# Kernel tuning notes

Hardware: AMD Instinct MI355X
Metric: run time of the kernel (lower is better)

## Reference

```python
import jax, jax.numpy as jnp
import numpy as np

EPS = 1e-5

def _layer_norm(x, w, b):
    mu = jnp.mean(x, axis=-1, keepdims=True)
    var = jnp.mean(jnp.square(x - mu), axis=-1, keepdims=True)
    return (x - mu) * jax.lax.rsqrt(var + EPS) * w + b

def setup_inputs() -> dict:
    key = jax.random.key(0)
    ks = jax.random.split(key, 8)
    B, S, D = 8, 2048, 1024
    image_features = jax.random.normal(ks[0], (B, S, D), dtype=jnp.float32)
    text_features = jax.random.normal(ks[1], (B, S, D), dtype=jnp.float32)
    ln_w = jnp.ones((D,), dtype=jnp.float32)
    ln_b = jnp.zeros((D,), dtype=jnp.float32)
    lim = 1.0 / np.sqrt(D)
    W_img = jax.random.uniform(ks[2], (D, D), minval=-lim, maxval=lim, dtype=jnp.float32)
    b_img = jax.random.uniform(ks[3], (D,), minval=-lim, maxval=lim, dtype=jnp.float32)
    W_txt = jax.random.uniform(ks[4], (D, D), minval=-lim, maxval=lim, dtype=jnp.float32)
    b_txt = jax.random.uniform(ks[5], (D,), minval=-lim, maxval=lim, dtype=jnp.float32)
    return {"image_features": image_features, "text_features": text_features,
            "ln_w": ln_w, "ln_b": ln_b, "W_img": W_img, "b_img": b_img,
            "W_txt": W_txt, "b_txt": b_txt}

def reference(image_features, text_features, ln_w, ln_b, W_img, b_img, W_txt, b_txt):
    D = image_features.shape[-1]
    scale = D ** (-0.5)
    image_norm = _layer_norm(image_features, ln_w, ln_b)
    text_norm = _layer_norm(text_features, ln_w, ln_b)
    # torch Linear: x @ W^T + b
    image_proj = jnp.einsum('bsd,ed->bse', image_norm, W_img) + b_img  # [B,Si,D]
    text_proj = jnp.einsum('btd,ed->bte', text_norm, W_txt) + b_txt    # [B,St,D]
    attn = jnp.einsum('bsd,btd->bst', image_proj, text_proj) * scale   # [B,Si,St]
    attn = jax.nn.softmax(attn, axis=-1)
    image_out = jnp.einsum('bst,btd->bsd', attn, text_proj)            # [B,Si,D]
    text_out = jnp.einsum('bst,bsd->btd', attn, image_proj)            # [B,St,D]
    return (image_out, text_out)
```

## Files before the change

kernel.cpp:

```cpp
#include <hip/hip_runtime.h>


#define DEV __device__ __forceinline__

typedef short s16x8 __attribute__((ext_vector_type(8)));
typedef float f32x4 __attribute__((ext_vector_type(4)));

DEV unsigned short f2bf(float f){
  unsigned u = __float_as_uint(f);
  u = (u + 0x7fffu + ((u >> 16) & 1u)) >> 16;
  return (unsigned short)u;
}
DEV float bf2f(unsigned short s){ return __uint_as_float(((unsigned)s) << 16); }

DEV void ldsload16(const void* g, void* l){
  __builtin_amdgcn_global_load_lds((const __attribute__((address_space(1))) void*)g,
                                   (__attribute__((address_space(3))) void*)l, 16, 0, 0);
}

__global__ __launch_bounds__(256) void k_cvt(const float* __restrict__ src,
                                             unsigned short* __restrict__ dst, int n4){
  int i = blockIdx.x * 256 + threadIdx.x;
  if (i < n4){
    float4 v = ((const float4*)src)[i];
    ushort4 o;
    o.x = f2bf(v.x); o.y = f2bf(v.y); o.z = f2bf(v.z); o.w = f2bf(v.w);
    ((ushort4*)dst)[i] = o;
  }
}

__global__ __launch_bounds__(256) void k_ln(const float* __restrict__ x,
                                            const float* __restrict__ w,
                                            const float* __restrict__ b,
                                            unsigned short* __restrict__ y){
  int row = blockIdx.x, tid = threadIdx.x;
  float4 v = ((const float4*)(x + (size_t)row * 1024))[tid];
  float s  = v.x + v.y + v.z + v.w;
  float s2 = v.x*v.x + v.y*v.y + v.z*v.z + v.w*v.w;
  #pragma unroll
  for (int o = 32; o > 0; o >>= 1){ s += __shfl_xor(s, o, 64); s2 += __shfl_xor(s2, o, 64); }
  __shared__ float sh[8];
  int wv = tid >> 6, ln = tid & 63;
  if (!ln){ sh[wv] = s; sh[4 + wv] = s2; }
  __syncthreads();
  s  = sh[0] + sh[1] + sh[2] + sh[3];
  s2 = sh[4] + sh[5] + sh[6] + sh[7];
  float mean = s * (1.f/1024.f);
  float var  = s2 * (1.f/1024.f) - mean * mean;
  float rstd = rsqrtf(var + 1e-5f);
  float4 w4 = ((const float4*)w)[tid];
  float4 b4 = ((const float4*)b)[tid];
  ushort4 o;
  o.x = f2bf((v.x-mean)*rstd*w4.x + b4.x);
  o.y = f2bf((v.y-mean)*rstd*w4.y + b4.y);
  o.z = f2bf((v.z-mean)*rstd*w4.z + b4.z);
  o.w = f2bf((v.w-mean)*rstd*w4.w + b4.w);
  ((ushort4*)(y + (size_t)row * 1024))[tid] = o;
}

#define STG(MAT, BASE, LD, T, H) do{                                              \
  ldsload16((BASE) + (size_t)(rl      ) * (LD) + (T)*64 + (H)*32 + g8,            \
            &MAT[(T)&1][H][(wave*16)*32]);                                        \
  ldsload16((BASE) + (size_t)(rl + 128) * (LD) + (T)*64 + (H)*32 + g8,            \
            &MAT[(T)&1][H][(128 + wave*16)*32]);                                  \
}while(0)

template<int OUT_BF16>
__global__ __launch_bounds__(512, 2) void k_gemm256(const unsigned short* __restrict__ A,
                                                    const unsigned short* __restrict__ Bt,
                                                    void* __restrict__ C,
                                                    const float* __restrict__ bias, float scale,
                                                    int K, int lda, int ldb, int ldc,
                                                    long sA, long sB, long sC,
                                                    int NBX, int NBY){
  __shared__ __align__(16) unsigned short As[2][2][8192];
  __shared__ __align__(16) unsigned short Bs[2][2][8192];
  int nwg = gridDim.x;
  int bid = blockIdx.x;
  int swz = (bid & 7) * (nwg >> 3) + (bid >> 3);
  int bx = swz % NBX; int rem = swz / NBX;
  int by = rem % NBY; int bz = rem / NBY;

  int tid = threadIdx.x, lane = tid & 63, wave = tid >> 6;
  int wm = wave >> 2, wn = wave & 3;
  int q = lane >> 4, fr = lane & 15;
  const unsigned short* Ab = A  + (size_t)bz * sA + (size_t)by * 256 * lda;
  const unsigned short* Bb = Bt + (size_t)bz * sB + (size_t)bx * 256 * ldb;
  int rl = wave*16 + (lane>>2);
  int g8 = (((lane&3) ^ ((lane>>2)&3) ^ ((lane>>4)&3))) * 8;
  int qp8 = ((q ^ (lane&3) ^ ((lane>>2)&3))) * 8;
  int aro = (wm*128 + fr)*32 + qp8;
  int bro = (wn*64  + fr)*32 + qp8;
  int NT = K >> 6, niter = K >> 7;

  f32x4 acc[8][4];
  #pragma unroll
  for (int m = 0; m < 8; ++m)
    #pragma unroll
    for (int n = 0; n < 4; ++n) acc[m][n] = f32x4{0.f, 0.f, 0.f, 0.f};

  STG(Bs, Bb, ldb, 0, 0);
  STG(As, Ab, lda, 0, 0);
  STG(Bs, Bb, ldb, 0, 1);
  STG(As, Ab, lda, 0, 1);
  asm volatile("s_waitcnt vmcnt(4)" ::: "memory");
  asm volatile("s_barrier" ::: "memory");

  for (int i = 0; i < niter; ++i){
    s16x8 bf[4];
    #pragma unroll
    for (int ph = 0; ph < 8; ++ph){
      const int buf = ph >> 2;
      const int kk  = (ph >> 1) & 1;
      const unsigned short* Ah = &As[buf][kk][0];
      const unsigned short* Bh = &Bs[buf][kk][0];
      s16x8 af[4];
      if ((ph & 1) == 0){
        #pragma unroll
        for (int n = 0; n < 4; ++n) bf[n] = *(const s16x8*)&Bh[bro + n*512];
        #pragma unroll
        for (int mi = 0; mi < 4; ++mi) af[mi] = *(const s16x8*)&Ah[aro + mi*512];
      } else {
        #pragma unroll
        for (int mi = 0; mi < 4; ++mi) af[mi] = *(const s16x8*)&Ah[aro + (4+mi)*512];
      }
      {
        int tgt = 2*i + ((ph < 4) ? 1 : 2);
        if (tgt < NT){
          const int h = (ph >> 1) & 1;
          if (ph & 1) STG(As, Ab, lda, tgt, h);
          else        STG(Bs, Bb, ldb, tgt, h);
        }
      }
      asm volatile("s_barrier" ::: "memory");
      asm volatile("s_waitcnt lgkmcnt(0)" ::: "memory");
      __builtin_amdgcn_s_setprio(1);
      #pragma unroll
      for (int mi = 0; mi < 4; ++mi)
        #pragma unroll
        for (int n = 0; n < 4; ++n)
          acc[(ph&1)*4 + mi][n] = __builtin_amdgcn_mfma_f32_16x16x32_bf16(
              af[mi], bf[n], acc[(ph&1)*4 + mi][n], 0, 0, 0);
      __builtin_amdgcn_s_setprio(0);
      if (ph & 1){
        if (i + 1 < niter || ph < 5)
          asm volatile("s_waitcnt vmcnt(4)" ::: "memory");
        else if (ph == 5)
          asm volatile("s_waitcnt vmcnt(0)" ::: "memory");
      }
      asm volatile("s_barrier" ::: "memory");
    }
  }
  size_t cb = (size_t)bz * sC;
  int row0 = by*256 + wm*128 + q*4;
  int col0 = bx*256 + wn*64 + fr;
  #pragma unroll
  for (int m = 0; m < 8; ++m){
    #pragma unroll
    for (int n = 0; n < 4; ++n){
      int col = col0 + n*16;
      float bv = bias ? bias[col] : 0.f;
      #pragma unroll
      for (int j = 0; j < 4; ++j){
        int row = row0 + m*16 + j;
        float vv = acc[m][n][j] * scale + bv;
        if (OUT_BF16) ((unsigned short*)C)[cb + (size_t)row*ldc + col] = f2bf(vv);
        else          ((float*)C)[cb + (size_t)row*ldc + col] = vv;
      }
    }
  }
}

__global__ __launch_bounds__(256) void k_transpose(const unsigned short* __restrict__ src,
                                                   unsigned short* __restrict__ dst,
                                                   int R, int C, long sS, long sD){
  __shared__ __align__(16) unsigned short tile[64 * 64];
  int tid = threadIdx.x;
  const unsigned short* sb = src + (size_t)blockIdx.z * sS;
  unsigned short* db = dst + (size_t)blockIdx.z * sD;
  int r0 = blockIdx.y * 64, c0 = blockIdx.x * 64;
  #pragma unroll
  for (int i = 0; i < 2; ++i){
    int ci = i * 256 + tid;
    int row = ci >> 3, cch = ci & 7;
    int pos = cch ^ (row & 7) ^ (row >> 3);
    uint4 v = *(const uint4*)&sb[(size_t)(r0 + row) * C + c0 + cch * 8];
    *(uint4*)&tile[row * 64 + pos * 8] = v;
  }
  __syncthreads();
  int ocp = tid >> 3, og = tid & 7;
  int oc = ocp * 2;
  union { uint4 v; unsigned short us[8]; } o0, o1;
  #pragma unroll
  for (int k = 0; k < 8; ++k){
    int r = og * 8 + k;
    int pos = (oc >> 3) ^ (r & 7) ^ (r >> 3);
    unsigned pr = *(const unsigned*)&tile[r * 64 + pos * 8 + (oc & 7)];
    o0.us[k] = (unsigned short)(pr & 0xffffu);
    o1.us[k] = (unsigned short)(pr >> 16);
  }
  *(uint4*)&db[(size_t)(c0 + oc    ) * R + r0 + og * 8] = o0.v;
  *(uint4*)&db[(size_t)(c0 + oc + 1) * R + r0 + og * 8] = o1.v;
}

__global__ __launch_bounds__(256) void k_softmax(unsigned short* __restrict__ a){
  size_t row = blockIdx.x;
  unsigned short* p = a + row * 2048;
  int tid = threadIdx.x;
  union { uint4 v; unsigned short us[8]; } in, out;
  in.v = *(const uint4*)&p[tid * 8];
  float x[8];
  #pragma unroll
  for (int j = 0; j < 8; ++j) x[j] = bf2f(in.us[j]);
  float mx = x[0];
  #pragma unroll
  for (int j = 1; j < 8; ++j) mx = fmaxf(mx, x[j]);
  #pragma unroll
  for (int o = 32; o > 0; o >>= 1) mx = fmaxf(mx, __shfl_xor(mx, o, 64));
  __shared__ float sh[8];
  int wv = tid >> 6, ln = tid & 63;
  if (!ln) sh[wv] = mx;
  __syncthreads();
  mx = fmaxf(fmaxf(sh[0], sh[1]), fmaxf(sh[2], sh[3]));
  float sm = 0.f, e[8];
  #pragma unroll
  for (int j = 0; j < 8; ++j){ e[j] = __expf(x[j] - mx); sm += e[j]; }
  #pragma unroll
  for (int o = 32; o > 0; o >>= 1) sm += __shfl_xor(sm, o, 64);
  if (!ln) sh[4 + wv] = sm;
  __syncthreads();
  sm = sh[4] + sh[5] + sh[6] + sh[7];
  float inv = 1.f / sm;
  #pragma unroll
  for (int j = 0; j < 8; ++j) out.us[j] = f2bf(e[j] * inv);
  *(uint4*)&p[tid * 8] = out.v;
}

extern "C" void kernel_launch(void* const* d_in, const int* in_sizes, int n_in,
                              void* d_out, int out_size, void* d_ws, size_t ws_size,
                              hipStream_t stream) {
  const float* img  = (const float*)d_in[0];
  const float* txt  = (const float*)d_in[1];
  const float* lnw  = (const float*)d_in[2];
  const float* lnb  = (const float*)d_in[3];
  const float* Wimg = (const float*)d_in[4];
  const float* bimg = (const float*)d_in[5];
  const float* Wtxt = (const float*)d_in[6];
  const float* btxt = (const float*)d_in[7];
  float* out = (float*)d_out;

  char* ws = (char*)d_ws;
  unsigned short* R1 = (unsigned short*)ws;
  unsigned short* R2 = (unsigned short*)(ws + 67108864);
  unsigned short* WB = (unsigned short*)(ws + 134217728);
  unsigned short* R4 = (unsigned short*)(ws + 138412032);

  const long PB = 2097152;
  const long AB = 4194304;

  k_cvt<<<1024, 256, 0, stream>>>(Wimg, WB,           262144);
  k_cvt<<<1024, 256, 0, stream>>>(Wtxt, WB + 1048576, 262144);
  k_ln<<<16384, 256, 0, stream>>>(img, lnw, lnb, R1);
  k_ln<<<16384, 256, 0, stream>>>(txt, lnw, lnb, R1 + 16777216);
  k_gemm256<1><<<256, 512, 0, stream>>>(R1,            WB,           R2,            bimg, 1.f,
                                        1024, 1024, 1024, 1024, 0, 0, 0, 4, 64);
  k_gemm256<1><<<256, 512, 0, stream>>>(R1 + 16777216, WB + 1048576, R2 + 16777216, btxt, 1.f,
                                        1024, 1024, 1024, 1024, 0, 0, 0, 4, 64);
  dim3 gt(16, 32, 8);
  k_transpose<<<gt, 256, 0, stream>>>(R2,            R1,            2048, 1024, PB, PB);
  k_transpose<<<gt, 256, 0, stream>>>(R2 + 16777216, R1 + 16777216, 2048, 1024, PB, PB);
  k_gemm256<1><<<512, 512, 0, stream>>>(R2, R2 + 16777216, R4, nullptr, 0.03125f,
                                        1024, 1024, 1024, 2048, PB, PB, AB, 8, 8);
  k_softmax<<<16384, 256, 0, stream>>>(R4);
  dim3 gat(32, 32, 8);
  k_transpose<<<gat, 256, 0, stream>>>(R4, R2, 2048, 2048, AB, AB);
  k_gemm256<0><<<256, 512, 0, stream>>>(R4, R1 + 16777216, out, nullptr, 1.f,
                                        2048, 2048, 2048, 1024, AB, PB, PB, 4, 8);
  k_gemm256<0><<<256, 512, 0, stream>>>(R2, R1, out + 16777216, nullptr, 1.f,
                                        2048, 2048, 2048, 1024, AB, PB, PB, 4, 8);
}
```

Measured before the change: 439.7 us.

## Relayout GEMM LDS tiles per 16-row fragment and deepen prefetch pipeline

Reorganizes the shared-memory tiles into per-16-row fragment blocks with a new XOR swizzle, changing both the global-to-LDS staging addresses and the fragment read offsets. The main loop now iterates per 64-wide K tile instead of per 128, and the prologue stages one and a half tiles ahead, with vmcnt thresholds adjusted so more loads stay in flight. The aim is fewer LDS bank conflicts and better hiding of global latency. The risk is swizzle correctness and more outstanding loads to track.

```diff
diff --git a/kernel.cpp b/kernel.cpp
--- a/kernel.cpp
+++ b/kernel.cpp
@@ -59,10 +59,10 @@
 }
 
 #define STG(MAT, BASE, LD, T, H) do{                                              \
-  ldsload16((BASE) + (size_t)(rl      ) * (LD) + (T)*64 + (H)*32 + g8,            \
-            &MAT[(T)&1][H][(wave*16)*32]);                                        \
-  ldsload16((BASE) + (size_t)(rl + 128) * (LD) + (T)*64 + (H)*32 + g8,            \
-            &MAT[(T)&1][H][(128 + wave*16)*32]);                                  \
+  ldsload16((BASE) + (size_t)(wave*16 + sfr) * (LD) + (T)*64 + (H)*32 + sq*8,     \
+            &MAT[(T)&1][H][wave][0]);                                             \
+  ldsload16((BASE) + (size_t)(wave*16 + 128 + sfr) * (LD) + (T)*64 + (H)*32 + sq*8,\
+            &MAT[(T)&1][H][wave + 8][0]);                                         \
 }while(0)
 
 template<int OUT_BF16>
@@ -73,8 +73,8 @@
                                                     int K, int lda, int ldb, int ldc,
                                                     long sA, long sB, long sC,
                                                     int NBX, int NBY){
-  __shared__ __align__(16) unsigned short As[2][2][8192];
-  __shared__ __align__(16) unsigned short Bs[2][2][8192];
+  __shared__ __align__(16) unsigned short As[2][2][16][512];
+  __shared__ __align__(16) unsigned short Bs[2][2][16][512];
   int nwg = gridDim.x;
   int bid = blockIdx.x;
   int swz = (bid & 7) * (nwg >> 3) + (bid >> 3);
@@ -86,12 +86,11 @@
   int q = lane >> 4, fr = lane & 15;
   const unsigned short* Ab = A  + (size_t)bz * sA + (size_t)by * 256 * lda;
   const unsigned short* Bb = Bt + (size_t)bz * sB + (size_t)bx * 256 * ldb;
-  int rl = wave*16 + (lane>>2);
-  int g8 = (((lane&3) ^ ((lane>>2)&3) ^ ((lane>>4)&3))) * 8;
-  int qp8 = ((q ^ (lane&3) ^ ((lane>>2)&3))) * 8;
-  int aro = (wm*128 + fr)*32 + qp8;
-  int bro = (wn*64  + fr)*32 + qp8;
-  int NT = K >> 6, niter = K >> 7;
+  int v   = (lane & 7) ^ ((lane >> 3) & 7);
+  int sfr = 2 * (lane >> 3) + (v >> 2);
+  int sq  = v & 3;
+  int roff = ((fr >> 1) << 6) + (((q + ((fr & 1) << 2)) ^ ((fr >> 1) & 7)) << 3);
+  int NT = K >> 6;
 
   f32x4 acc[8][4];
   #pragma unroll
@@ -99,39 +98,34 @@
     #pragma unroll
     for (int n = 0; n < 4; ++n) acc[m][n] = f32x4{0.f, 0.f, 0.f, 0.f};
 
-  STG(Bs, Bb, ldb, 0, 0);
-  STG(As, Ab, lda, 0, 0);
-  STG(Bs, Bb, ldb, 0, 1);
-  STG(As, Ab, lda, 0, 1);
-  asm volatile("s_waitcnt vmcnt(4)" ::: "memory");
+  STG(As, Ab, lda, 0, 0); STG(Bs, Bb, ldb, 0, 0);
+  STG(As, Ab, lda, 0, 1); STG(Bs, Bb, ldb, 0, 1);
+  STG(As, Ab, lda, 1, 0); STG(Bs, Bb, ldb, 1, 0);
+  asm volatile("s_waitcnt vmcnt(8)" ::: "memory");
   asm volatile("s_barrier" ::: "memory");
 
-  for (int i = 0; i < niter; ++i){
-    s16x8 bf[4];
+  for (int t = 0; t < NT; ++t){
+    const int buf = t & 1;
+    s16x8 bfr[4];
     #pragma unroll
-    for (int ph = 0; ph < 8; ++ph){
-      const int buf = ph >> 2;
-      const int kk  = (ph >> 1) & 1;
-      const unsigned short* Ah = &As[buf][kk][0];
-      const unsigned short* Bh = &Bs[buf][kk][0];
+    for (int ph = 0; ph < 4; ++ph){
+      const int kk = ph >> 1;
+      const unsigned short* Ah = &As[buf][kk][0][0];
+      const unsigned short* Bh = &Bs[buf][kk][0][0];
       s16x8 af[4];
       if ((ph & 1) == 0){
         #pragma unroll
-        for (int n = 0; n < 4; ++n) bf[n] = *(const s16x8*)&Bh[bro + n*512];
-        #pragma unroll
-        for (int mi = 0; mi < 4; ++mi) af[mi] = *(const s16x8*)&Ah[aro + mi*512];
+        for (int n = 0; n < 4; ++n)  bfr[n] = *(const s16x8*)&Bh[(wn*4 + n)*512 + roff];
+        #pragma unroll
+        for (int mi = 0; mi < 4; ++mi) af[mi] = *(const s16x8*)&Ah[(wm*8 + mi)*512 + roff];
       } else {
         #pragma unroll
-        for (int mi = 0; mi < 4; ++mi) af[mi] = *(const s16x8*)&Ah[aro + (4+mi)*512];
+        for (int mi = 0; mi < 4; ++mi) af[mi] = *(const s16x8*)&Ah[(wm*8 + 4 + mi)*512 + roff];
       }
-      {
-        int tgt = 2*i + ((ph < 4) ? 1 : 2);
-        if (tgt < NT){
-          const int h = (ph >> 1) & 1;
-          if (ph & 1) STG(As, Ab, lda, tgt, h);
-          else        STG(Bs, Bb, ldb, tgt, h);
-        }
-      }
+      if (ph == 0){ if (t + 1 < NT) STG(As, Ab, lda, t + 1, 1); }
+      if (ph == 1){ if (t + 1 < NT) STG(Bs, Bb, ldb, t + 1, 1); }
+      if (ph == 2){ if (t + 2 < NT) STG(As, Ab, lda, t + 2, 0); }
+      if (ph == 3){ if (t + 2 < NT) STG(Bs, Bb, ldb, t + 2, 0); }
       asm volatile("s_barrier" ::: "memory");
       asm volatile("s_waitcnt lgkmcnt(0)" ::: "memory");
       __builtin_amdgcn_s_setprio(1);
@@ -140,13 +134,11 @@
         #pragma unroll
         for (int n = 0; n < 4; ++n)
           acc[(ph&1)*4 + mi][n] = __builtin_amdgcn_mfma_f32_16x16x32_bf16(
-              af[mi], bf[n], acc[(ph&1)*4 + mi][n], 0, 0, 0);
+              af[mi], bfr[n], acc[(ph&1)*4 + mi][n], 0, 0, 0);
       __builtin_amdgcn_s_setprio(0);
       if (ph & 1){
-        if (i + 1 < niter || ph < 5)
-          asm volatile("s_waitcnt vmcnt(4)" ::: "memory");
-        else if (ph == 5)
-          asm volatile("s_waitcnt vmcnt(0)" ::: "memory");
+        if (t + 2 < NT) asm volatile("s_waitcnt vmcnt(8)" ::: "memory");
+        else            asm volatile("s_waitcnt vmcnt(0)" ::: "memory");
       }
       asm volatile("s_barrier" ::: "memory");
     }
```

Result: faster. 422.7 us (-3.9%).
